# Performance work log

Measured on AMD Instinct MI355X. Metric: run time of the kernel, lower is better.

The kernel has to match this reference:

```python
import jax, jax.numpy as jnp
import numpy as np
jax.config.update("jax_enable_x64", True)  # need >32-bit lattice-key packing

D = 5          # feature dim
B_OFF = 1024   # coordinate offset for integer key packing
BASE = 2 * B_OFF


def _encode(keys):
    # keys: [..., D] int32 lattice coords (first D of the D+1 zero-sum coords)
    code = jnp.zeros(keys.shape[:-1], jnp.int64)
    for i in range(D):
        code = code * BASE + (keys[..., i].astype(jnp.int64) + B_OFF)
    return code


def _decode(code):
    coords = []
    c = code
    for _ in range(D):
        coords.append((c % BASE) - B_OFF)
        c = c // BASE
    return jnp.stack(coords[::-1], axis=-1).astype(jnp.int32)


def _lattice_filter(feature, values):
    """Permutohedral lattice filter: splat -> (d+1) directional blurs -> slice."""
    N, d = feature.shape
    vd = values.shape[1]
    f = feature.astype(jnp.float32)
    vals = values.astype(jnp.float32)

    # ---- elevate features onto the hyperplane H_{d+1} (Adams et al. E matrix) ----
    inv_std = np.sqrt(2.0 / 3.0) * (d + 1)
    scale = jnp.asarray(inv_std / np.sqrt(np.arange(1, d + 1) * np.arange(2, d + 2)),
                        jnp.float32)
    c = f * scale                                        # [N, d]
    S = jnp.cumsum(c[:, ::-1], axis=1)[:, ::-1]          # suffix sums: S[:,i] = sum c[:,i:]
    suffix = jnp.concatenate([S[:, 1:], jnp.zeros((N, 1), c.dtype)], axis=1)
    idx = jnp.arange(1, d + 1, dtype=c.dtype)
    elevated = jnp.concatenate([S[:, :1], suffix - idx * c], axis=1)   # [N, d+1]

    # ---- nearest zero-colored lattice point (multiples of d+1) ----
    down = 1.0 / (d + 1)
    rd = jnp.round(elevated * down)
    rem0 = rd * (d + 1)
    sum_ = jnp.sum(rd, axis=1).astype(jnp.int32)
    diff = (elevated - rem0) * down
    order = jnp.argsort(-diff, axis=1, stable=True)
    rank = jnp.argsort(order, axis=1).astype(jnp.int32) + sum_[:, None]
    rem0i = rem0.astype(jnp.int32)
    shift = (rank < 0).astype(jnp.int32) - (rank > d).astype(jnp.int32)
    rank = rank + (d + 1) * shift
    rem0i = rem0i + (d + 1) * shift

    # ---- barycentric coordinates ----
    t = (elevated - rem0i.astype(elevated.dtype)) * down
    rows = jnp.arange(N)[:, None]
    b = jnp.zeros((N, d + 2), elevated.dtype)
    b = b.at[rows, d - rank].add(t)
    b = b.at[rows, d + 1 - rank].add(-t)
    b0 = b[:, 0] + 1.0 + b[:, d + 1]
    bary = jnp.concatenate([b0[:, None], b[:, 1:d + 1]], axis=1)        # [N, d+1]

    # ---- keys of the d+1 enclosing simplex vertices (store first d coords) ----
    r = jnp.arange(d + 1, dtype=jnp.int32)
    canonical = jnp.where(rank[:, None, :] >= (d + 1 - r)[None, :, None],
                          r[None, :, None] - (d + 1), r[None, :, None])  # [N,d+1,d+1]
    keys = rem0i[:, None, :d] + canonical[..., :d]                       # [N,d+1,d]

    # ---- hash + unique lattice vertices (fixed-size for jit) ----
    M = N * (d + 1)
    codes = _encode(keys.reshape(M, d))
    FILL = jnp.iinfo(jnp.int64).max
    uniq = jnp.unique(codes, size=M, fill_value=FILL)   # sorted, padded
    inv = jnp.searchsorted(uniq, codes)

    # ---- splat ----
    contrib = (bary[:, :, None] * vals[:, None, :]).reshape(M, vd)
    val = jax.ops.segment_sum(contrib, inv, num_segments=M)             # [M, vd]

    # ---- blur along each of the d+1 lattice directions ([1,2,1]/4 kernel) ----
    coords = _decode(uniq)                                              # [M, d]
    full = jnp.concatenate([coords, -jnp.sum(coords, axis=1, keepdims=True)], axis=1)
    for j in range(d + 1):
        off = jnp.ones((d + 1,), jnp.int32).at[j].set(-d)

        def look(nk, cur):
            cde = _encode(nk[:, :d])
            ii = jnp.clip(jnp.searchsorted(uniq, cde), 0, M - 1)
            ok = uniq[ii] == cde
            return jnp.where(ok[:, None], cur[ii], 0.0)

        val = 0.5 * val + 0.25 * (look(full + off, val) + look(full - off, val))

    # ---- slice ----
    alpha = 1.0 / (1.0 + 2.0 ** (-d))
    sliced = val[inv].reshape(N, d + 1, vd)
    return alpha * jnp.einsum('nr,nrv->nv', bary, sliced)


def setup_inputs() -> dict:
    key = jax.random.key(0)
    k1, k2 = jax.random.split(key)
    N = 1 << 20
    feature = jax.random.normal(k1, (N, D), dtype=jnp.float32)
    values = jax.random.normal(k2, (N, 16), dtype=jnp.float32)
    return {"feature": feature, "values": values}


def reference(feature, values):
    return _lattice_filter(feature, values)
```

## Files before the change

### kernel.cpp

```cpp
#include <hip/hip_runtime.h>
#include <stdint.h>

typedef unsigned long long u64;
typedef unsigned int u32;
typedef unsigned short u16;

static constexpr u64 KEMPTY = ~0ull;
static constexpr int PROBE_CAP = 32768;
static constexpr u32 BINS  = 4096;
static constexpr u32 CHUNK = 4096;
static constexpr u32 SPLIT = 2048;

static constexpr u32 THRESH = 23040;
static constexpr u32 UMAXR  = 23040;
static constexpr u32 S1     = 16;

static __device__ __forceinline__ u64 mix64(u64 x){
  x ^= x >> 30; x *= 0xbf58476d1ce4e5b9ull;
  x ^= x >> 27; x *= 0x94d049bb133111ebull;
  x ^= x >> 31; return x;
}

static __device__ __forceinline__ long long lookup_slot(const u64* __restrict__ tk, u32 cmask, u64 code){
  u32 h = (u32)mix64(code) & cmask;
#pragma unroll 1
  for(int p=0;p<PROBE_CAP;p++){
    u64 cur = tk[h];
    if(cur==code) return (long long)h;
    if(cur==KEMPTY) return -1;
    h=(h+1)&cmask;
  }
  return -1;
}

static __device__ __forceinline__ void atomAddF(float* p, float v){
#if defined(__gfx90a__) || defined(__gfx940__) || defined(__gfx941__) || defined(__gfx942__) || defined(__gfx950__)
  unsafeAtomicAdd(p, v);
#else
  atomicAdd(p, v);
#endif
}

static __device__ __forceinline__ void lds_add(float* p, float v){
  __hip_atomic_fetch_add(p, v, __ATOMIC_RELAXED, __HIP_MEMORY_SCOPE_WORKGROUP);
}
static __device__ __forceinline__ void lds_addu(u32* p, u32 v){
  __hip_atomic_fetch_add(p, v, __ATOMIC_RELAXED, __HIP_MEMORY_SCOPE_WORKGROUP);
}
static __device__ __forceinline__ u32 lds_addu_rtn(u32* p, u32 v){
  return __hip_atomic_fetch_add(p, v, __ATOMIC_RELAXED, __HIP_MEMORY_SCOPE_WORKGROUP);
}

static __device__ __forceinline__ void row_load(const float* __restrict__ p, float* o){
  const float4* q=(const float4*)p;
#pragma unroll
  for(int i=0;i<4;i++){ float4 v=q[i]; o[4*i]=v.x; o[4*i+1]=v.y; o[4*i+2]=v.z; o[4*i+3]=v.w; }
}
static __device__ __forceinline__ void row_store(float* __restrict__ p, const float* o){
  float4* q=(float4*)p;
#pragma unroll
  for(int i=0;i<4;i++) q[i]=make_float4(o[4*i],o[4*i+1],o[4*i+2],o[4*i+3]);
}

__global__ void __launch_bounds__(256)
k_setup(const float* __restrict__ feat, int N,
        u64* __restrict__ tabk, u32 cmask,
        u32* __restrict__ inv_slot, float* __restrict__ baryT)
{
#pragma clang fp contract(off)
  int n = blockIdx.x*256 + threadIdx.x;
  if(n>=N) return;

  const float s0=3.4641016151377544f, s1=2.0f, s2=1.4142135623730951f,
              s3=1.0954451150103321f, s4=0.8944271909999159f;
  float c[5];
  c[0]=feat[n*5+0]*s0; c[1]=feat[n*5+1]*s1; c[2]=feat[n*5+2]*s2;
  c[3]=feat[n*5+3]*s3; c[4]=feat[n*5+4]*s4;

  float sfx[6]; sfx[5]=0.f;
#pragma unroll
  for(int i=4;i>=0;i--) sfx[i]=sfx[i+1]+c[i];
  float el[6];
  el[0]=sfx[0];
#pragma unroll
  for(int i=1;i<6;i++) el[i]=sfx[i]-(float)i*c[i-1];

  const float down=1.0f/6.0f;
  float rd[6], rem0[6], rdsum=0.f;
#pragma unroll
  for(int i=0;i<6;i++){ rd[i]=rintf(el[i]*down); rem0[i]=rd[i]*6.0f; rdsum+=rd[i]; }
  int sumi=(int)rdsum;

  float diff[6];
#pragma unroll
  for(int i=0;i<6;i++) diff[i]=(el[i]-rem0[i])*down;

  int rank[6];
#pragma unroll
  for(int i=0;i<6;i++){
    int r=0;
#pragma unroll
    for(int j=0;j<6;j++)
      r += (diff[j]>diff[i]) || (diff[j]==diff[i] && j<i);
    rank[i]=r+sumi;
  }
  int rem0i[6];
#pragma unroll
  for(int i=0;i<6;i++){
    rem0i[i]=(int)rem0[i];
    int sh=(rank[i]<0)-(rank[i]>5);
    rank[i]+=6*sh; rem0i[i]+=6*sh;
  }

  float b[7]={0.f,0.f,0.f,0.f,0.f,0.f,0.f};
#pragma unroll
  for(int i=0;i<6;i++){
    float t=(el[i]-(float)rem0i[i])*down;
    int k0=5-rank[i]; if(k0>=0&&k0<7) b[k0]+=t;
  }
#pragma unroll
  for(int i=0;i<6;i++){
    float t=(el[i]-(float)rem0i[i])*down;
    int k1=6-rank[i]; if(k1>=0&&k1<7) b[k1]-=t;
  }
  baryT[n]=(b[0]+1.0f)+b[6];
#pragma unroll
  for(int r=1;r<6;r++) baryT[(size_t)r*N+n]=b[r];

#pragma unroll 1
  for(int r=0;r<6;r++){
    long long code=0;
#pragma unroll
    for(int i=0;i<5;i++){
      int key = rem0i[i] + ((rank[i] >= 6-r) ? (r-6) : r);
      code = code*2048 + (long long)(key+1024);
    }
    u32 h=(u32)mix64((u64)code)&cmask;
    u32 slot=0xFFFFFFFFu;
#pragma unroll 1
    for(int p=0;p<PROBE_CAP;p++){
      u64 cur=tabk[h];
      if(cur==(u64)code){ slot=h; break; }
      if(cur==KEMPTY){
        u64 old=atomicCAS((unsigned long long*)&tabk[h], KEMPTY, (u64)code);
        if(old==KEMPTY || old==(u64)code){ slot=h; break; }
      } else {
        h=(h+1)&cmask;
      }
    }
    inv_slot[(size_t)r*N+n]=slot;
  }
}

__global__ void __launch_bounds__(256)
k_uid(const u64* __restrict__ tabk, u32 C, u32 Ucap, u32* __restrict__ tuid,
      u32* __restrict__ uidslot, u32* __restrict__ counter)
{
  u32 s=blockIdx.x*256+threadIdx.x;
  if(s>=C) return;
  if(tabk[s]==KEMPTY) return;
  u32 uid=atomicAdd(counter,1u);
  if(uid<Ucap) uidslot[uid]=s; else uid=0;
  tuid[s]=uid;
}

__global__ void __launch_bounds__(256)
k_translate(u32* __restrict__ inv, u16* __restrict__ inv16,
            const u32* __restrict__ tuid, size_t M)
{
  size_t i=(size_t)blockIdx.x*256+threadIdx.x;
  if(i<M){
    u32 u=tuid[inv[i]];
    inv[i]=u;
    inv16[i]=(u16)u;
  }
}

__global__ void __launch_bounds__(256)
k_vtrans(const float* __restrict__ values, float* __restrict__ valuesT, int N)
{
  __shared__ float tile[256][17];
  u32 b=blockIdx.x, t=threadIdx.x;
  size_t p=(size_t)b*256+t;
  float v[16];
  row_load(values+p*16, v);
#pragma unroll
  for(int k=0;k<16;k++) tile[t][k]=v[k];
  __syncthreads();
  u32 ch=t>>4, lane=t&15;
#pragma unroll
  for(int q=0;q<16;q++){
    u32 pt=q*16+lane;
    valuesT[(size_t)ch*N + (size_t)b*256 + pt]=tile[pt][ch];
  }
}

__global__ void __launch_bounds__(1024, 1)
k_saccum1(const u16* __restrict__ inv16, const float* __restrict__ baryT,
          const float* __restrict__ valuesT, const u32* __restrict__ counter,
          int N, float* __restrict__ partial1)
{
  __shared__ float acc1[THRESH];
  u32 U=*counter;
  if(U>THRESH) return;
  u32 j=blockIdx.x;
  u32 cs=j&15, sub=j>>4;
  u32 t=threadIdx.x;
  for(u32 x=t;x<U;x+=1024) acc1[x]=0.f;
  __syncthreads();

  u32 nsub=(u32)N/S1;
  size_t p0=(size_t)sub*nsub;
  const float* vch=valuesT+(size_t)cs*N;
  for(u32 i=t;i<nsub;i+=1024){
    size_t p=p0+i;
    float v=vch[p];
#pragma unroll
    for(int r=0;r<6;r++){
      u32 u=inv16[(size_t)r*N+p];
      float w=baryT[(size_t)r*N+p];
      lds_add(&acc1[u], w*v);
    }
  }
  __syncthreads();
  float* dst=partial1+(size_t)j*UMAXR;
  for(u32 x=t;x<U;x+=1024) dst[x]=acc1[x];
}

__global__ void __launch_bounds__(256)
k_reduce1(const float* __restrict__ partial1, const u32* __restrict__ counter,
          float* __restrict__ v0)
{
  u32 U=*counter;
  if(U>THRESH) return;
  u32 cs=blockIdx.y;
  u32 u=blockIdx.x*256+threadIdx.x;
  if(u>=U) return;
  float s=0.f;
#pragma unroll
  for(u32 sub=0;sub<S1;sub++)
    s+=partial1[(size_t)(sub*16+cs)*UMAXR+u];
  v0[(size_t)u*16+cs]=s;
}

__global__ void __launch_bounds__(256)
k_hist(const u32* __restrict__ inv, const u32* __restrict__ counter,
       u32* __restrict__ hist, size_t M)
{
  if(*counter<=THRESH) return;
  __shared__ u32 h[BINS];
  u32 t=threadIdx.x, b=blockIdx.x;
#pragma unroll
  for(int j=0;j<(int)(BINS/256);j++) h[t+j*256]=0;
  __syncthreads();
  size_t base=(size_t)b*CHUNK;
#pragma unroll
  for(int j=0;j<(int)(CHUNK/256);j++){
    size_t i=base + (size_t)j*256 + t;
    if(i<M){
      u32 u=inv[i];
      lds_addu(&h[u&(BINS-1)],1u);
    }
  }
  __syncthreads();
#pragma unroll
  for(int j=0;j<(int)(BINS/256);j++){
    u32 bin=t+j*256;
    hist[(size_t)b*BINS+bin]=h[bin];
  }
}

__global__ void __launch_bounds__(256)
k_transpose(const u32* __restrict__ in, u32* __restrict__ out, u32 R, u32 C,
            const u32* __restrict__ counter)
{
  if(*counter<=THRESH) return;
  __shared__ u32 tile[32][33];
  u32 bx=blockIdx.x, by=blockIdx.y;
  u32 tx=threadIdx.x&31, ty=threadIdx.x>>5;
  u32 c0=bx*32, r0=by*32;
#pragma unroll
  for(u32 j=0;j<32;j+=8){
    u32 r=r0+ty+j, c=c0+tx;
    if(r<R && c<C) tile[ty+j][tx]=in[(size_t)r*C+c];
  }
  __syncthreads();
#pragma unroll
  for(u32 j=0;j<32;j+=8){
    u32 c=c0+ty+j, r=r0+tx;
    if(c<C && r<R) out[(size_t)c*R+r]=tile[tx][ty+j];
  }
}

__global__ void __launch_bounds__(256)
k_scan1(const u32* __restrict__ v, u32* __restrict__ bsum, const u32* __restrict__ counter)
{
  if(*counter<=THRESH) return;
  __shared__ u32 sm[256];
  u32 t=threadIdx.x, b=blockIdx.x;
  size_t base=((size_t)b*256+t)*4;
  u32 s=v[base]+v[base+1]+v[base+2]+v[base+3];
  sm[t]=s; __syncthreads();
  for(int o=128;o>0;o>>=1){ if(t<(u32)o) sm[t]+=sm[t+o]; __syncthreads(); }
  if(t==0) bsum[b]=sm[0];
}

__global__ void __launch_bounds__(256)
k_scan2(u32* __restrict__ bsum, u32 nb, const u32* __restrict__ counter)
{
  if(*counter<=THRESH) return;
  __shared__ u32 sm[256];
  u32 t=threadIdx.x;
  u32 per=(nb+255)/256;
  u32 lo=t*per, hi=lo+per; if(hi>nb) hi=nb; if(lo>nb) lo=nb;
  u32 tot=0;
  for(u32 i=lo;i<hi;i++) tot+=bsum[i];
  sm[t]=tot; __syncthreads();
  for(int o=1;o<256;o<<=1){
    u32 v=sm[t]; u32 a=(t>=(u32)o)?sm[t-o]:0u; __syncthreads();
    sm[t]=v+a; __syncthreads();
  }
  u32 run=sm[t]-tot;
  for(u32 i=lo;i<hi;i++){ u32 c=bsum[i]; bsum[i]=run; run+=c; }
}

__global__ void __launch_bounds__(256)
k_scan3(u32* __restrict__ v, const u32* __restrict__ bsum, const u32* __restrict__ counter)
{
  if(*counter<=THRESH) return;
  __shared__ u32 sm[256];
  u32 t=threadIdx.x, b=blockIdx.x;
  size_t base=((size_t)b*256+t)*4;
  u32 c[4]; u32 tot=0;
#pragma unroll
  for(int j=0;j<4;j++){ c[j]=v[base+j]; tot+=c[j]; }
  sm[t]=tot; __syncthreads();
  for(int o=1;o<256;o<<=1){
    u32 x=sm[t]; u32 a=(t>=(u32)o)?sm[t-o]:0u; __syncthreads();
    sm[t]=x+a; __syncthreads();
  }
  u32 run=bsum[b]+sm[t]-tot;
#pragma unroll
  for(int j=0;j<4;j++){ v[base+j]=run; run+=c[j]; }
}

__global__ void __launch_bounds__(256)
k_part(const u32* __restrict__ inv, const float* __restrict__ baryT,
       const u32* __restrict__ histT, u32 nb,
       u32* __restrict__ skey, float* __restrict__ sw, size_t M, u32 nmask,
       const u32* __restrict__ counter)
{
  if(*counter<=THRESH) return;
  __shared__ u32 cur[BINS];
  u32 t=threadIdx.x, b=blockIdx.x;
#pragma unroll
  for(int j=0;j<(int)(BINS/256);j++){
    u32 bin=t+j*256;
    cur[bin]=histT[(size_t)bin*nb+b];
  }
  __syncthreads();
  size_t base=(size_t)b*CHUNK;
#pragma unroll
  for(int j=0;j<(int)(CHUNK/256);j++){
    size_t i=base+(size_t)j*256+t;
    if(i<M){
      u32 u=inv[i];
      u32 pos=lds_addu_rtn(&cur[u&(BINS-1)],1u);
      skey[pos]=((u>>12)<<20)|((u32)i & nmask);
      sw[pos]=baryT[i];
    }
  }
}

__global__ void __launch_bounds__(256)
k_queue(const u32* __restrict__ histT, u32 nb, size_t M,
        u32* __restrict__ q, u32* __restrict__ qn, const u32* __restrict__ counter)
{
  if(*counter<=THRESH) return;
  u32 b=blockIdx.x*256+threadIdx.x;
  if(b>=BINS) return;
  size_t s=histT[(size_t)b*nb];
  size_t e=(b+1<BINS)? (size_t)histT[(size_t)(b+1)*nb] : M;
  u32 sz=(u32)(e-s);
  if(sz==0) return;
  u32 G=(sz+SPLIT-1)/SPLIT; if(G>1023u) G=1023u;
  u32 base=atomicAdd(qn,G);
  for(u32 g=0; g<G; g++) q[base+g] = b | (g<<12) | (G<<22);
}

__global__ void __launch_bounds__(256)
k_accum(const u32* __restrict__ q, const u32* __restrict__ qn,
        const u32* __restrict__ skey, const float* __restrict__ sw,
        const float* __restrict__ values, const u32* __restrict__ histT,
        u32 nb, u32 rows, size_t M, float* __restrict__ v0)
{
  __shared__ float acc[4352];
  u32 j=blockIdx.x;
  if(j>=*qn) return;
  u32 ent=q[j];
  u32 b=ent&4095u, g=(ent>>12)&1023u, G=ent>>22;
  size_t s0=histT[(size_t)b*nb];
  size_t e0=(b+1<BINS)? (size_t)histT[(size_t)(b+1)*nb] : M;
  u32 sz=(u32)(e0-s0);
  u32 chunk=(sz+G-1)/G;
  size_t s=s0+(size_t)g*chunk;
  size_t e=s+chunk; if(e>e0) e=e0;

  u32 t=threadIdx.x;
  for(u32 x=t;x<rows*17;x+=256) acc[x]=0.f;
  __syncthreads();

  if(G==1){
    size_t base=s;
    for(; base+512<=e; base+=512){
      size_t i0=base+t, i1=base+256+t;
      u32 key0=skey[i0], key1=skey[i1];
      float w0=sw[i0], w1=sw[i1];
      float r0[16], r1[16];
      row_load(values+(size_t)(key0&0xFFFFFu)*16, r0);
      row_load(values+(size_t)(key1&0xFFFFFu)*16, r1);
      u32 a0=(key0>>20)*17, a1=(key1>>20)*17;
#pragma unroll
      for(int k=0;k<16;k++) lds_add(&acc[a0+k], w0*r0[k]);
#pragma unroll
      for(int k=0;k<16;k++) lds_add(&acc[a1+k], w1*r1[k]);
    }
    for(; base<e; base+=256){
      size_t ei=base+t;
      if(ei<e){
        u32 key=skey[ei]; float w=sw[ei];
        float r[16];
        row_load(values+(size_t)(key&0xFFFFFu)*16, r);
        u32 a=(key>>20)*17;
#pragma unroll
        for(int k=0;k<16;k++) lds_add(&acc[a+k], w*r[k]);
      }
    }
  } else {
    u32 gr=t>>4, k=t&15;
    size_t base=s;
    for(; base+128<=e; base+=128){
      u32 key[8]; float w[8]; float x[8];
#pragma unroll
      for(int u8=0;u8<8;u8++){ size_t ei=base+(size_t)u8*16+gr; key[u8]=skey[ei]; w[u8]=sw[ei]; }
#pragma unroll
      for(int u8=0;u8<8;u8++){ x[u8]=values[(size_t)(key[u8]&0xFFFFFu)*16+k]; }
#pragma unroll
      for(int u8=0;u8<8;u8++) lds_add(&acc[(key[u8]>>20)*17+k], w[u8]*x[u8]);
    }
    for(; base<e; base+=16){
      size_t ei=base+gr;
      if(ei<e){
        u32 key=skey[ei]; float w=sw[ei];
        float x=values[(size_t)(key&0xFFFFFu)*16+k];
        lds_add(&acc[(key>>20)*17+k], w*x);
      }
    }
  }
  __syncthreads();

  if(G==1){
    for(u32 x=t;x<rows*16;x+=256){
      u32 row=x>>4, kk=x&15;
      v0[(size_t)((row<<12)|b)*16+kk]=acc[row*17+kk];
    }
  } else {
    for(u32 x=t;x<rows*16;x+=256){
      u32 row=x>>4, kk=x&15;
      float a=acc[row*17+kk];
      if(a!=0.f) atomAddF(&v0[(size_t)((row<<12)|b)*16+kk], a);
    }
  }
}

__global__ void __launch_bounds__(256)
k_blur(const u64* __restrict__ tabk, const u32* __restrict__ tuid, u32 cmask,
       const u32* __restrict__ uidslot, const u32* __restrict__ counter, u32 Ucap,
       long long delta, const float* __restrict__ vin, float* __restrict__ vout)
{
  u32 m=blockIdx.x*256+threadIdx.x;
  u32 U=*counter; if(U>Ucap) U=Ucap;
  if(m>=U) return;
  long long code=(long long)tabk[uidslot[m]];
  long long sp=lookup_slot(tabk,cmask,(u64)(code+delta));
  long long sm=lookup_slot(tabk,cmask,(u64)(code-delta));
  float acc[16];
  row_load(vin+(size_t)m*16, acc);
#pragma unroll
  for(int k=0;k<16;k++) acc[k]*=0.5f;
  if(sp>=0){
    u32 u=tuid[sp]; float t[16]; row_load(vin+(size_t)u*16,t);
#pragma unroll
    for(int k=0;k<16;k++) acc[k]+=0.25f*t[k];
  }
  if(sm>=0){
    u32 u=tuid[sm]; float t[16]; row_load(vin+(size_t)u*16,t);
#pragma unroll
    for(int k=0;k<16;k++) acc[k]+=0.25f*t[k];
  }
  row_store(vout+(size_t)m*16, acc);
}

__global__ void __launch_bounds__(256)
k_slice(const u32* __restrict__ inv, const float* __restrict__ baryT,
        const float* __restrict__ val, int N, float* __restrict__ out)
{
  int n=blockIdx.x*256+threadIdx.x;
  if(n>=N) return;
  u32 u[6]; float w[6];
#pragma unroll
  for(int r=0;r<6;r++){ u[r]=inv[(size_t)r*N+n]; w[r]=baryT[(size_t)r*N+n]; }
  float t6[6][16];
#pragma unroll
  for(int r=0;r<6;r++) row_load(val+(size_t)u[r]*16, t6[r]);
  float acc[16];
#pragma unroll
  for(int k=0;k<16;k++){
    float a=w[0]*t6[0][k];
#pragma unroll
    for(int r=1;r<6;r++) a+=w[r]*t6[r][k];
    acc[k]=a;
  }
  const float alpha=0.9696969696969697f;
  float4* q=(float4*)(out+(size_t)n*16);
#pragma unroll
  for(int i=0;i<4;i++) q[i]=make_float4(alpha*acc[4*i],alpha*acc[4*i+1],alpha*acc[4*i+2],alpha*acc[4*i+3]);
}

__global__ void k_diag(float* out, float v){ out[0]=v; }

extern "C" void kernel_launch(void* const* d_in, const int* in_sizes, int n_in,
                              void* d_out, int out_size, void* d_ws, size_t ws_size,
                              hipStream_t stream)
{
  const float* feat   =(const float*)d_in[0];
  const float* values =(const float*)d_in[1];
  float* out=(float*)d_out;
  int N=in_sizes[0]/5;
  size_t M=(size_t)N*6;
  u32 nmask=(u32)(N-1);

  u32 nb=(u32)((M+CHUNK-1)/CHUNK);
  size_t K=(size_t)nb*BINS;
  const u32 QCAP=16384;

  size_t part_scratch = K*4+K*4+M*4+M*4+(K/1024)*4+QCAP*4+1024;
  size_t vt_bytes     = (size_t)N*16*4;
  size_t partial1b    = (size_t)256*UMAXR*4;
  auto v1bytes=[&](size_t U)->size_t{
    size_t m1=U*64;
    if(part_scratch>m1) m1=part_scratch;
    if(vt_bytes+partial1b>m1) m1=vt_bytes+partial1b;
    return m1;
  };
  auto need=[&](int lC,int lU)->size_t{
    size_t C=1ull<<lC, U=1ull<<lU, s=0;
    auto al=[&](size_t b){ s=(s+255)&~(size_t)255; s+=b; };
    al(4); al(M*4); al(M*4); al(M*2); al(C*8); al(C*4); al(U*4); al(U*64); al(v1bytes(U));
    return s+256;
  };
  const int prefs[3][2]={{21,20},{21,19},{20,18}};
  int lC=0,lU=0;
  for(int i=0;i<3;i++){ if(need(prefs[i][0],prefs[i][1])<=ws_size){ lC=prefs[i][0]; lU=prefs[i][1]; break; } }
  if(!lC){
    hipMemsetAsync(d_out,0,(size_t)out_size*sizeof(float),stream);
    k_diag<<<1,1,0,stream>>>(out,(float)(ws_size>>20));
    return;
  }

  size_t C=1ull<<lC, Ucap=1ull<<lU; u32 cmask=(u32)(C-1);
  char* base=(char*)d_ws; size_t offb=0;
  auto carve=[&](size_t b)->char*{ offb=(offb+255)&~(size_t)255; char* p=base+offb; offb+=b; return p; };
  u32*   counter=(u32*)carve(4);
  u32*   inv    =(u32*)carve(M*4);
  float* baryT  =(float*)carve(M*4);
  u16*   inv16  =(u16*)carve(M*2);
  u64*   tabk   =(u64*)carve(C*8);
  u32*   tuid   =(u32*)carve(C*4);
  u32*   uidslot=(u32*)carve(Ucap*4);
  float* v0     =(float*)carve(Ucap*64);
  float* v1     =(float*)carve(v1bytes(Ucap));

  u32*   hist =(u32*)v1;
  u32*   histT=hist+K;
  u32*   skey =histT+K;
  float* sw   =(float*)(skey+M);
  u32*   bsum =(u32*)(sw+M);
  u32*   q    =bsum+(K/1024);
  u32*   qn   =q+QCAP;
  float* valuesT =(float*)v1;
  float* partial1=(float*)((char*)v1+vt_bytes);

  hipMemsetAsync(counter,0,4,stream);
  hipMemsetAsync(tabk,0xFF,C*8,stream);
  hipMemsetAsync(v0,0,Ucap*64,stream);

  const int B=256;
  k_setup    <<<(N+B-1)/B,B,0,stream>>>(feat,N,tabk,cmask,inv,baryT);
  k_uid      <<<(u32)((C+B-1)/B),B,0,stream>>>(tabk,(u32)C,(u32)Ucap,tuid,uidslot,counter);
  k_translate<<<(u32)((M+B-1)/B),B,0,stream>>>(inv,inv16,tuid,M);

  k_vtrans <<<(u32)(N/256),B,0,stream>>>(values,valuesT,N);
  k_saccum1<<<16*S1,1024,0,stream>>>(inv16,baryT,valuesT,counter,N,partial1);
  {
    dim3 g((THRESH+B-1)/B,16);
    k_reduce1<<<g,B,0,stream>>>(partial1,counter,v0);
  }

  hipMemsetAsync(qn,0,4,stream);
  k_hist <<<nb,B,0,stream>>>(inv,counter,hist,M);
  {
    dim3 g((BINS+31)/32,(nb+31)/32);
    k_transpose<<<g,B,0,stream>>>(hist,histT,nb,BINS,counter);
  }
  u32 sb=(u32)(K/1024);
  k_scan1<<<sb,B,0,stream>>>(histT,bsum,counter);
  k_scan2<<<1 ,B,0,stream>>>(bsum,sb,counter);
  k_scan3<<<sb,B,0,stream>>>(histT,bsum,counter);
  k_part <<<nb,B,0,stream>>>(inv,baryT,histT,nb,skey,sw,M,nmask,counter);
  k_queue<<<(BINS+B-1)/B,B,0,stream>>>(histT,nb,M,q,qn,counter);
  u32 rows=(u32)(Ucap>>12);
  k_accum<<<QCAP,B,0,stream>>>(q,qn,skey,sw,values,histT,nb,rows,M,v0);

  const long long P[5]={1ll,2048ll,1ll<<22,1ll<<33,1ll<<44};
  const long long SUM=P[0]+P[1]+P[2]+P[3]+P[4];
  u32 gb=(u32)((Ucap+B-1)/B);
  float* a=v0; float* bb=v1;
  for(int j=0;j<6;j++){
    long long delta=(j<5)? (SUM-6*P[4-j]) : SUM;
    k_blur<<<gb,B,0,stream>>>(tabk,tuid,cmask,uidslot,counter,(u32)Ucap,delta,a,bb);
    float* t=a; a=bb; bb=t;
  }
  k_slice<<<(N+B-1)/B,B,0,stream>>>(inv,baryT,a,N,out);
}
```

Measured before the change: 1.057 ms.

## Split splat accumulation into small-LDS and large-LDS variants with vectorized loads

Replaces the single LDS splat kernel with two variants chosen at runtime by the unique-vertex count. When the count fits a smaller shared array, a kernel with 512 blocks, a smaller LDS footprint and float4/ushort4 loads runs, so more blocks can be resident per CU. Otherwise a kernel with software-prefetched float2 loads runs. The reduce kernel now handles both partial layouts, and the hash table size preference is halved, which lowers memset and scan cost but raises the load factor and probe lengths.

Result: no change. 1.038 ms (-1.8%).

```diff
diff --git a/kernel.cpp b/kernel.cpp
--- a/kernel.cpp
+++ b/kernel.cpp
@@ -13,7 +13,7 @@
 
 static constexpr u32 THRESH = 23040;
 static constexpr u32 UMAXR  = 23040;
-static constexpr u32 S1     = 16;
+static constexpr u32 USM    = 12672;
 
 static __device__ __forceinline__ u64 mix64(u64 x){
   x ^= x >> 30; x *= 0xbf58476d1ce4e5b9ull;
@@ -195,32 +195,96 @@
   }
 }
 
-__global__ void __launch_bounds__(1024, 1)
-k_saccum1(const u16* __restrict__ inv16, const float* __restrict__ baryT,
-          const float* __restrict__ valuesT, const u32* __restrict__ counter,
-          int N, float* __restrict__ partial1)
-{
-  __shared__ float acc1[THRESH];
+__global__ void __launch_bounds__(1024, 8)
+k_saccum1s(const u16* __restrict__ inv16, const float* __restrict__ baryT,
+           const float* __restrict__ valuesT, const u32* __restrict__ counter,
+           int N, float* __restrict__ partial1)
+{
+  __shared__ float acc1[USM];
   u32 U=*counter;
-  if(U>THRESH) return;
+  if(U>USM) return;
   u32 j=blockIdx.x;
   u32 cs=j&15, sub=j>>4;
   u32 t=threadIdx.x;
   for(u32 x=t;x<U;x+=1024) acc1[x]=0.f;
   __syncthreads();
 
-  u32 nsub=(u32)N/S1;
+  u32 nsub=(u32)N/32;
+  u32 quads=nsub>>2;
   size_t p0=(size_t)sub*nsub;
   const float* vch=valuesT+(size_t)cs*N;
-  for(u32 i=t;i<nsub;i+=1024){
-    size_t p=p0+i;
-    float v=vch[p];
+  for(u32 q=t;q<quads;q+=1024){
+    size_t p=p0+(size_t)q*4;
+    float4 v=*(const float4*)(vch+p);
 #pragma unroll
     for(int r=0;r<6;r++){
-      u32 u=inv16[(size_t)r*N+p];
-      float w=baryT[(size_t)r*N+p];
-      lds_add(&acc1[u], w*v);
-    }
+      ushort4 uu=*(const ushort4*)(inv16+(size_t)r*N+p);
+      float4  w =*(const float4*)(baryT+(size_t)r*N+p);
+      lds_add(&acc1[uu.x], w.x*v.x);
+      lds_add(&acc1[uu.y], w.y*v.y);
+      lds_add(&acc1[uu.z], w.z*v.z);
+      lds_add(&acc1[uu.w], w.w*v.w);
+    }
+  }
+  __syncthreads();
+  float* dst=partial1+(size_t)j*USM;
+  for(u32 x=t;x<U;x+=1024) dst[x]=acc1[x];
+}
+
+__global__ void __launch_bounds__(1024, 4)
+k_saccum1b(const u16* __restrict__ inv16, const float* __restrict__ baryT,
+           const float* __restrict__ valuesT, const u32* __restrict__ counter,
+           int N, float* __restrict__ partial1)
+{
+  __shared__ float acc1[THRESH];
+  u32 U=*counter;
+  if(U<=USM || U>THRESH) return;
+  u32 j=blockIdx.x;
+  u32 cs=j&15, sub=j>>4;
+  u32 t=threadIdx.x;
+  for(u32 x=t;x<U;x+=1024) acc1[x]=0.f;
+  __syncthreads();
+
+  u32 nsub=(u32)N/16;
+  u32 pairs=nsub>>1;
+  u32 iters=pairs/1024;
+  size_t p0=(size_t)sub*nsub;
+  const float* vch=valuesT+(size_t)cs*N;
+
+  u32 q=t;
+  float2 vA=make_float2(0.f,0.f); ushort2 uA[6]; float2 wA[6];
+  {
+    size_t p=p0+(size_t)q*2;
+    vA=*(const float2*)(vch+p);
+#pragma unroll
+    for(int r=0;r<6;r++){
+      uA[r]=*(const ushort2*)(inv16+(size_t)r*N+p);
+      wA[r]=*(const float2*)(baryT+(size_t)r*N+p);
+    }
+  }
+  for(u32 it=0;it<iters;++it){
+    u32 qn2=q+1024;
+    float2 vB=make_float2(0.f,0.f); ushort2 uB[6]; float2 wB[6];
+#pragma unroll
+    for(int r=0;r<6;r++){ uB[r]=make_ushort2(0,0); wB[r]=make_float2(0.f,0.f); }
+    if(it+1<iters){
+      size_t pn=p0+(size_t)qn2*2;
+      vB=*(const float2*)(vch+pn);
+#pragma unroll
+      for(int r=0;r<6;r++){
+        uB[r]=*(const ushort2*)(inv16+(size_t)r*N+pn);
+        wB[r]=*(const float2*)(baryT+(size_t)r*N+pn);
+      }
+    }
+#pragma unroll
+    for(int r=0;r<6;r++){
+      lds_add(&acc1[uA[r].x], wA[r].x*vA.x);
+      lds_add(&acc1[uA[r].y], wA[r].y*vA.y);
+    }
+    vA=vB;
+#pragma unroll
+    for(int r=0;r<6;r++){ uA[r]=uB[r]; wA[r]=wB[r]; }
+    q=qn2;
   }
   __syncthreads();
   float* dst=partial1+(size_t)j*UMAXR;
@@ -233,13 +297,15 @@
 {
   u32 U=*counter;
   if(U>THRESH) return;
+  bool small=(U<=USM);
+  u32 S = small?32u:16u;
+  size_t stride = small?(size_t)USM:(size_t)UMAXR;
   u32 cs=blockIdx.y;
   u32 u=blockIdx.x*256+threadIdx.x;
   if(u>=U) return;
   float s=0.f;
-#pragma unroll
-  for(u32 sub=0;sub<S1;sub++)
-    s+=partial1[(size_t)(sub*16+cs)*UMAXR+u];
+  for(u32 sub=0;sub<S;sub++)
+    s+=partial1[(size_t)(sub*16+cs)*stride+u];
   v0[(size_t)u*16+cs]=s;
 }
 
@@ -546,7 +612,8 @@
 
   size_t part_scratch = K*4+K*4+M*4+M*4+(K/1024)*4+QCAP*4+1024;
   size_t vt_bytes     = (size_t)N*16*4;
-  size_t partial1b    = (size_t)256*UMAXR*4;
+  size_t partial1b    = (size_t)512*USM*4;
+  if((size_t)256*UMAXR*4>partial1b) partial1b=(size_t)256*UMAXR*4;
   auto v1bytes=[&](size_t U)->size_t{
     size_t m1=U*64;
     if(part_scratch>m1) m1=part_scratch;
@@ -559,7 +626,7 @@
     al(4); al(M*4); al(M*4); al(M*2); al(C*8); al(C*4); al(U*4); al(U*64); al(v1bytes(U));
     return s+256;
   };
-  const int prefs[3][2]={{21,20},{21,19},{20,18}};
+  const int prefs[3][2]={{20,20},{20,19},{19,18}};
   int lC=0,lU=0;
   for(int i=0;i<3;i++){ if(need(prefs[i][0],prefs[i][1])<=ws_size){ lC=prefs[i][0]; lU=prefs[i][1]; break; } }
   if(!lC){
@@ -600,8 +667,9 @@
   k_uid      <<<(u32)((C+B-1)/B),B,0,stream>>>(tabk,(u32)C,(u32)Ucap,tuid,uidslot,counter);
   k_translate<<<(u32)((M+B-1)/B),B,0,stream>>>(inv,inv16,tuid,M);
 
-  k_vtrans <<<(u32)(N/256),B,0,stream>>>(values,valuesT,N);
-  k_saccum1<<<16*S1,1024,0,stream>>>(inv16,baryT,valuesT,counter,N,partial1);
+  k_vtrans  <<<(u32)(N/256),B,0,stream>>>(values,valuesT,N);
+  k_saccum1s<<<512,1024,0,stream>>>(inv16,baryT,valuesT,counter,N,partial1);
+  k_saccum1b<<<256,1024,0,stream>>>(inv16,baryT,valuesT,counter,N,partial1);
   {
     dim3 g((THRESH+B-1)/B,16);
     k_reduce1<<<g,B,0,stream>>>(partial1,counter,v0);
```
